# Kernel optimization log

Hardware: AMD Instinct MI355X
Metric: run time of the kernel (lower is better)

Reference implementation:

```python
import jax, jax.numpy as jnp
import numpy as np

UNITS = 14336
IN_FEATURES = 4096
PACKED = IN_FEATURES // 4  # 4 ternary values (2 bits each) per byte
CLIP_VAL = 100.0

# 2-bit crumb -> ternary value lookup: 0 -> 0, 1 -> +1, 2 -> -1, 3 -> 0
_TERNARY_LUT = jnp.array([0.0, 1.0, -1.0, 0.0], dtype=jnp.float32)


def _unpack_ternary(pw):
    """pw: [U, P] int (byte values 0..255) -> dense ternary float W [U, 4*P].
    Little-endian crumbs within each byte (shifts 0,2,4,6)."""
    crumbs = jnp.stack([(pw >> (2 * i)) & 3 for i in range(4)], axis=-1)  # [U, P, 4]
    crumbs = crumbs.reshape(pw.shape[0], -1)  # [U, 4*P]
    return _TERNARY_LUT[crumbs][:, :IN_FEATURES]  # [U, IN]


def setup_inputs() -> dict:
    key = jax.random.key(0)
    k1, k2, k3, k4 = jax.random.split(key, 4)
    x = jax.random.normal(k1, (32, IN_FEATURES), dtype=jnp.float32)
    # packed ternary weights, one uint8-valued byte per 4 ternary weights
    pw = jax.random.randint(k2, (UNITS, PACKED), 0, 256, dtype=jnp.int32)
    scale = 1.0 + 0.02 * jax.random.normal(k3, (UNITS,), dtype=jnp.float32)
    bias = 0.01 * jax.random.normal(k4, (UNITS,), dtype=jnp.float32)
    return {"x": x, "pw": pw, "scale": scale, "bias": bias}


def reference(x, pw, scale, bias):
    # dense ternary weight [UNITS, IN]; kernel target would fuse this unpack into the GEMM
    W = _unpack_ternary(pw)
    y = jnp.einsum('bd,ud->bu', x, W)  # [B, UNITS]
    y = y * scale + bias               # per-unit affine dequant
    return jnp.clip(y, -CLIP_VAL, CLIP_VAL)
```

## Files before the change

### kernel.cpp

```cpp
#include <hip/hip_runtime.h>

#define UNITS 14336
#define IN_F 4096
#define PACKED 1024
#define CLIP_VAL 100.0f

typedef unsigned int uint32;

using bf16x8 = __attribute__((ext_vector_type(8))) short;
using f32x4  = __attribute__((ext_vector_type(4))) float;

__device__ inline unsigned short f2bf(float f) {
    uint32 u = __float_as_uint(f);
    u += 0x7FFFu + ((u >> 16) & 1u);
    return (unsigned short)(u >> 16);
}

__device__ inline uint32 pack2bf(float a, float b) {
    return (uint32)f2bf(a) | ((uint32)f2bf(b) << 16);
}

__device__ inline void unpack_byte(int v, uint32& r0, uint32& r1) {
    uint32 t0 = ((uint32)v & 3u) | (((uint32)v & 0xCu) << 14);
    uint32 t1 = (((uint32)v >> 4) & 3u) | (((uint32)v & 0xC0u) << 10);
    uint32 s0 = t0 >> 1;
    uint32 s1 = t1 >> 1;
    uint32 nz0 = (t0 ^ s0) & 0x00010001u;
    uint32 nz1 = (t1 ^ s1) & 0x00010001u;
    r0 = nz0 * 0x3F80u + ((s0 & 0x00010001u) << 15);
    r1 = nz1 * 0x3F80u + ((s1 & 0x00010001u) << 15);
}

__device__ inline float clipf(float y) {
    return fminf(fmaxf(y, -CLIP_VAL), CLIP_VAL);
}


__global__ __launch_bounds__(256) void convert_x_kernel(
    const float* __restrict__ x, uint4* __restrict__ ws) {
    int t = blockIdx.x * 256 + threadIdx.x;
    int lane = t & 63;
    int h = (t >> 6) & 1;
    int s = (t >> 7) & 1;
    int g = t >> 8;
    int n = lane & 15;
    int q = lane >> 4;
    int b = h * 16 + n;
    int k0 = g * 64 + q * 16 + s * 8;
    const float4* src = (const float4*)(x + (size_t)b * IN_F + k0);
    float4 lo = src[0];
    float4 hi = src[1];
    uint4 o;
    o.x = pack2bf(lo.x, lo.y);
    o.y = pack2bf(lo.z, lo.w);
    o.z = pack2bf(hi.x, hi.y);
    o.w = pack2bf(hi.z, hi.w);
    ws[t] = o;
}

__global__ __launch_bounds__(1024, 8) void ternary_mm_kernel(
    const uint4* __restrict__ xw,
    const int*   __restrict__ pw,
    const float* __restrict__ scale,
    const float* __restrict__ bias,
    float*       __restrict__ out) {
    __shared__ f32x4 red[16][2][64];

    const int tid  = threadIdx.x;
    const int wid  = tid >> 6;
    const int lane = tid & 63;
    const int q    = lane >> 4;
    const int n    = lane & 15;
    const int u0   = blockIdx.x << 4;

    f32x4 acc0 = {0.f,0.f,0.f,0.f};
    f32x4 acc1 = {0.f,0.f,0.f,0.f};

    const int g0 = wid << 2;
    const int*   pA = pw + (size_t)(u0 + n) * PACKED + (g0 << 4) + (q << 2);
    const uint4* xb = xw + (g0 << 8) + lane;

    #pragma unroll
    for (int i = 0; i < 4; ++i) {
        int4 w4 = *(const int4*)(pA + (i << 4));
        uint4 x00 = xb[(i << 8)];
        uint4 x01 = xb[(i << 8) + 64];
        uint4 x10 = xb[(i << 8) + 128];
        uint4 x11 = xb[(i << 8) + 192];

        uint4 fA, fB;
        unpack_byte(w4.x, fA.x, fA.y);
        unpack_byte(w4.y, fA.z, fA.w);
        unpack_byte(w4.z, fB.x, fB.y);
        unpack_byte(w4.w, fB.z, fB.w);
        bf16x8 vA = __builtin_bit_cast(bf16x8, fA);
        bf16x8 vB = __builtin_bit_cast(bf16x8, fB);

        acc0 = __builtin_amdgcn_mfma_f32_16x16x32_bf16(
            __builtin_bit_cast(bf16x8, x00), vA, acc0, 0, 0, 0);
        acc1 = __builtin_amdgcn_mfma_f32_16x16x32_bf16(
            __builtin_bit_cast(bf16x8, x01), vA, acc1, 0, 0, 0);
        acc0 = __builtin_amdgcn_mfma_f32_16x16x32_bf16(
            __builtin_bit_cast(bf16x8, x10), vB, acc0, 0, 0, 0);
        acc1 = __builtin_amdgcn_mfma_f32_16x16x32_bf16(
            __builtin_bit_cast(bf16x8, x11), vB, acc1, 0, 0, 0);
    }

    red[wid][0][lane] = acc0;
    red[wid][1][lane] = acc1;
    __syncthreads();

    if (tid < 128) {
        const int h = tid >> 6;
        const int l = tid & 63;
        f32x4 s = red[0][h][l];
        #pragma unroll
        for (int w = 1; w < 16; ++w) {
            f32x4 v = red[w][h][l];
            s[0] += v[0]; s[1] += v[1]; s[2] += v[2]; s[3] += v[3];
        }
        const int u  = u0 + (l & 15);
        const int b0 = h * 16 + ((l >> 4) << 2);
        const float sc = scale[u];
        const float bi = bias[u];
        float* o = out + (size_t)b0 * UNITS + u;
        o[0 * UNITS] = clipf(s[0] * sc + bi);
        o[1 * UNITS] = clipf(s[1] * sc + bi);
        o[2 * UNITS] = clipf(s[2] * sc + bi);
        o[3 * UNITS] = clipf(s[3] * sc + bi);
    }
}

extern "C" void kernel_launch(void* const* d_in, const int* in_sizes, int n_in,
                              void* d_out, int out_size, void* d_ws, size_t ws_size,
                              hipStream_t stream) {
    const float* x     = (const float*)d_in[0];
    const int*   pw    = (const int*)d_in[1];
    const float* scale = (const float*)d_in[2];
    const float* bias  = (const float*)d_in[3];
    float* out = (float*)d_out;

    uint4* xw = (uint4*)d_ws;

    convert_x_kernel<<<64, 256, 0, stream>>>(x, xw);
    ternary_mm_kernel<<<UNITS / 16, 1024, 0, stream>>>(xw, pw, scale, bias, out);
}
```

Measured before the change: 105.7 us.

## Stage packed weights via global_load_lds, replicate x per XCD, prefetch x

Weight tiles for each block are now loaded directly into LDS with global_load_lds in coalesced row chunks, replacing strided per-lane global int4 loads. The bf16 copy of x is written 8 times, once per blockIdx%8 group, so each XCD reads its own copy and stays within its local L2. x fragments are software-prefetched one iteration ahead. The reduction buffer reuses the same LDS, which adds an extra barrier, and the convert kernel launch grows 8x.

```diff
diff --git a/kernel.cpp b/kernel.cpp
--- a/kernel.cpp
+++ b/kernel.cpp
@@ -38,16 +38,18 @@
 
 __global__ __launch_bounds__(256) void convert_x_kernel(
     const float* __restrict__ x, uint4* __restrict__ ws) {
-    int t = blockIdx.x * 256 + threadIdx.x;
+    int b = blockIdx.x;
+    int c = b & 7;
+    int t = ((b >> 3) << 8) + threadIdx.x;
     int lane = t & 63;
     int h = (t >> 6) & 1;
     int s = (t >> 7) & 1;
     int g = t >> 8;
     int n = lane & 15;
     int q = lane >> 4;
-    int b = h * 16 + n;
+    int bi = h * 16 + n;
     int k0 = g * 64 + q * 16 + s * 8;
-    const float4* src = (const float4*)(x + (size_t)b * IN_F + k0);
+    const float4* src = (const float4*)(x + (size_t)bi * IN_F + k0);
     float4 lo = src[0];
     float4 hi = src[1];
     uint4 o;
@@ -55,7 +57,7 @@
     o.y = pack2bf(lo.z, lo.w);
     o.z = pack2bf(hi.x, hi.y);
     o.w = pack2bf(hi.z, hi.w);
-    ws[t] = o;
+    ws[c * 16384 + t] = o;
 }
 
 __global__ __launch_bounds__(1024, 8) void ternary_mm_kernel(
@@ -64,29 +66,45 @@
     const float* __restrict__ scale,
     const float* __restrict__ bias,
     float*       __restrict__ out) {
-    __shared__ f32x4 red[16][2][64];
+    __shared__ int lds[16384];
 
     const int tid  = threadIdx.x;
     const int wid  = tid >> 6;
     const int lane = tid & 63;
-    const int q    = lane >> 4;
-    const int n    = lane & 15;
     const int u0   = blockIdx.x << 4;
+    const int g0   = wid << 2;
+
+    {
+        const char* srcb = (const char*)(pw + (size_t)u0 * PACKED)
+                         + (lane & 15) * 4096 + ((lane >> 4) << 4);
+        #pragma unroll
+        for (int t = 0; t < 4; ++t) {
+            const int g = g0 + t;
+            __builtin_amdgcn_global_load_lds(
+                (const __attribute__((address_space(1))) uint32*)(srcb + (g << 6)),
+                (__attribute__((address_space(3))) uint32*)(lds + (g << 8)),
+                16, 0, 0);
+        }
+    }
+
+    const uint4* xb = xw + ((blockIdx.x & 7) * 16384) + (g0 << 8) + lane;
+    uint4 xa0 = xb[0], xa1 = xb[64], xa2 = xb[128], xa3 = xb[192];
+
+    __builtin_amdgcn_s_waitcnt(0);
+    __builtin_amdgcn_sched_barrier(0);
 
     f32x4 acc0 = {0.f,0.f,0.f,0.f};
     f32x4 acc1 = {0.f,0.f,0.f,0.f};
-
-    const int g0 = wid << 2;
-    const int*   pA = pw + (size_t)(u0 + n) * PACKED + (g0 << 4) + (q << 2);
-    const uint4* xb = xw + (g0 << 8) + lane;
+    const char* lb = (const char*)lds + (lane << 4);
 
     #pragma unroll
     for (int i = 0; i < 4; ++i) {
-        int4 w4 = *(const int4*)(pA + (i << 4));
-        uint4 x00 = xb[(i << 8)];
-        uint4 x01 = xb[(i << 8) + 64];
-        uint4 x10 = xb[(i << 8) + 128];
-        uint4 x11 = xb[(i << 8) + 192];
+        uint4 xn0, xn1, xn2, xn3;
+        if (i < 3) {
+            const uint4* xi = xb + ((i + 1) << 8);
+            xn0 = xi[0]; xn1 = xi[64]; xn2 = xi[128]; xn3 = xi[192];
+        }
+        int4 w4 = *(const int4*)(lb + ((g0 + i) << 10));
 
         uint4 fA, fB;
         unpack_byte(w4.x, fA.x, fA.y);
@@ -97,26 +115,30 @@
         bf16x8 vB = __builtin_bit_cast(bf16x8, fB);
 
         acc0 = __builtin_amdgcn_mfma_f32_16x16x32_bf16(
-            __builtin_bit_cast(bf16x8, x00), vA, acc0, 0, 0, 0);
+            __builtin_bit_cast(bf16x8, xa0), vA, acc0, 0, 0, 0);
         acc1 = __builtin_amdgcn_mfma_f32_16x16x32_bf16(
-            __builtin_bit_cast(bf16x8, x01), vA, acc1, 0, 0, 0);
+            __builtin_bit_cast(bf16x8, xa1), vA, acc1, 0, 0, 0);
         acc0 = __builtin_amdgcn_mfma_f32_16x16x32_bf16(
-            __builtin_bit_cast(bf16x8, x10), vB, acc0, 0, 0, 0);
+            __builtin_bit_cast(bf16x8, xa2), vB, acc0, 0, 0, 0);
         acc1 = __builtin_amdgcn_mfma_f32_16x16x32_bf16(
-            __builtin_bit_cast(bf16x8, x11), vB, acc1, 0, 0, 0);
+            __builtin_bit_cast(bf16x8, xa3), vB, acc1, 0, 0, 0);
+
+        if (i < 3) { xa0 = xn0; xa1 = xn1; xa2 = xn2; xa3 = xn3; }
     }
 
-    red[wid][0][lane] = acc0;
-    red[wid][1][lane] = acc1;
+    __syncthreads();
+    f32x4* red = (f32x4*)lds;
+    red[(wid * 2 + 0) * 64 + lane] = acc0;
+    red[(wid * 2 + 1) * 64 + lane] = acc1;
     __syncthreads();
 
     if (tid < 128) {
         const int h = tid >> 6;
         const int l = tid & 63;
-        f32x4 s = red[0][h][l];
+        f32x4 s = red[h * 64 + l];
         #pragma unroll
         for (int w = 1; w < 16; ++w) {
-            f32x4 v = red[w][h][l];
+            f32x4 v = red[(w * 2 + h) * 64 + l];
             s[0] += v[0]; s[1] += v[1]; s[2] += v[2]; s[3] += v[3];
         }
         const int u  = u0 + (l & 15);
@@ -142,6 +164,6 @@
 
     uint4* xw = (uint4*)d_ws;
 
-    convert_x_kernel<<<64, 256, 0, stream>>>(x, xw);
+    convert_x_kernel<<<512, 256, 0, stream>>>(x, xw);
     ternary_mm_kernel<<<UNITS / 16, 1024, 0, stream>>>(xw, pw, scale, bias, out);
 }
```

Measured after the change: 107.4 us. Within noise of the previous version (+1.6%).
